# Performance work log

Hardware: AMD Instinct MI355X
Metric: run time of the kernel (lower is better)

Reference implementation:

```python
import jax, jax.numpy as jnp
import numpy as np

T = 16000        # signal length
N1 = 120         # first-order filters (J=12, Q=10)
NPSI2 = 14       # second-order filterbank size (Q2=1)
NPAIR = 553      # second-order coefficients -> 120 + 553 = 673 channels
SUB1 = 8         # subsample U1 before order 2
T2 = T // SUB1   # 2000
STR1 = 1000      # lowpass stride at length T  -> 16 output samples
STR2 = T2 // (T // STR1)  # 125 -> 16 output samples
LOG_EPS = 1e-6
BN_EPS = 1e-5


def _gauss_hat(N, xi, sigma):
    om = np.arange(N) / N
    return np.exp(-((om - xi) ** 2) / (2.0 * sigma ** 2)).astype(np.float32)


def _filterbank():
    Q = 10.0
    xi1 = 0.45 * 2.0 ** (-np.arange(N1) / Q)
    sig1 = np.maximum(xi1 * 0.1, 2.0 / T)
    psi1 = np.stack([_gauss_hat(T, x, s) for x, s in zip(xi1, sig1)])
    phi1 = _gauss_hat(T, 0.0, 0.4 / STR1)
    xi2 = 0.45 * 2.0 ** (-np.arange(NPSI2, dtype=np.float64))
    sig2 = np.maximum(xi2 * 0.2, 2.0 / T2)
    psi2 = np.stack([_gauss_hat(T2, x, s) for x, s in zip(xi2, sig2)])
    phi2 = _gauss_hat(T2, 0.0, 0.4 / STR2)
    pairs = [(i, j) for i in range(N1) for j in range(NPSI2) if xi2[j] < xi1[i] / 2.0]
    pairs = pairs[:NPAIR]
    assert len(pairs) == NPAIR
    pi1 = np.array([p[0] for p in pairs], np.int32)
    pi2 = np.array([p[1] for p in pairs], np.int32)
    return psi1, phi1, psi2, phi2, pi1, pi2


def setup_inputs():
    key = jax.random.key(0)
    ks = jax.random.split(key, 8)
    psi1, phi1, psi2, phi2, pi1, pi2 = _filterbank()
    B = 32
    inp = {
        "x": jax.random.normal(ks[0], (B, 1, T), jnp.float32),
        "psi1_hat": jnp.asarray(psi1),
        "phi1_hat": jnp.asarray(phi1),
        "psi2_hat": jnp.asarray(psi2),
        "phi2_hat": jnp.asarray(phi2),
        "gamma": jnp.ones((673,), jnp.float32),
        "beta": jnp.zeros((673,), jnp.float32),
        "W1": jax.random.normal(ks[1], (300, 673), jnp.float32) * 0.04,
        "b1": jnp.zeros((300,), jnp.float32),
        "W2": jax.random.normal(ks[2], (90, 300), jnp.float32) * 0.06,
        "b2": jnp.zeros((90,), jnp.float32),
        "W3": jax.random.normal(ks[3], (35, 90), jnp.float32) * 0.1,
        "b3": jnp.zeros((35,), jnp.float32),
        "pair_i1": jnp.asarray(pi1),
        "pair_i2": jnp.asarray(pi2),
    }
    return inp


def reference(x, psi1_hat, phi1_hat, psi2_hat, phi2_hat, gamma, beta,
              W1, b1, W2, b2, W3, b3, pair_i1, pair_i2):
    xs = x.squeeze(1)                                       # [B, T]
    Xf = jnp.fft.fft(xs)                                    # [B, T] c64
    # --- order 1: wavelet conv (freq-domain), modulus ---
    U1 = jnp.abs(jnp.fft.ifft(Xf[:, None, :] * psi1_hat[None]))        # [B, N1, T]
    # S1 = lowpass(U1) subsampled to 16 samples
    S1 = jnp.real(jnp.fft.ifft(jnp.fft.fft(U1) * phi1_hat))[..., ::STR1]  # [B, N1, 16]
    # --- order 2 on subsampled U1 ---
    U1sf = jnp.fft.fft(U1[..., ::SUB1])                     # [B, N1, T2]
    U2 = jnp.abs(jnp.fft.ifft(U1sf[:, pair_i1, :] * psi2_hat[pair_i2]))  # [B, NPAIR, T2]
    S2 = jnp.real(jnp.fft.ifft(jnp.fft.fft(U2) * phi2_hat))[..., ::STR2]  # [B, NPAIR, 16]
    S = jnp.concatenate([S1, S2], axis=1)                   # [B, 673, 16]
    # log-abs + temporal mean pooling
    f = jnp.mean(jnp.log(jnp.abs(S) + LOG_EPS), axis=-1)    # [B, 673]
    # BatchNorm1d (training mode: batch statistics)
    mu = jnp.mean(f, axis=0)
    var = jnp.var(f, axis=0)
    f = (f - mu) / jnp.sqrt(var + BN_EPS) * gamma + beta
    # MLP head
    h = jax.nn.relu(f @ W1.T + b1)
    h = jax.nn.relu(h @ W2.T + b2)
    return jax.nn.log_softmax(h @ W3.T + b3, axis=-1)
```

## Files before the change

kernel.cpp:

```cpp
#include <hip/hip_runtime.h>
#include <math.h>

typedef float2 cf;

__device__ __forceinline__ cf cadd(cf a, cf b){ return make_float2(a.x+b.x, a.y+b.y); }
__device__ __forceinline__ cf csub(cf a, cf b){ return make_float2(a.x-b.x, a.y-b.y); }
__device__ __forceinline__ cf cmul(cf a, cf b){ return make_float2(a.x*b.x - a.y*b.y, a.x*b.y + a.y*b.x); }

__device__ __forceinline__ int SW(int i){ return i ^ ((i>>4)&15); }
#define AT(x) s[SW(x)]
#define WFENCE asm volatile("" ::: "memory")


template<int N, int L, bool INV>
__device__ __forceinline__ void stage_r2(cf* __restrict__ s, const cf* __restrict__ tw, int tid, int nt){
  constexpr int Ls = L/2, nbf = N/2, tws = 16000/L;
  for (int q = tid; q < nbf; q += nt){
    int blk = q / Ls, j = q - blk*Ls;
    int base = blk*L + j;
    cf w1 = tw[tws*j]; if (INV) w1.y = -w1.y;
    if (!INV){
      cf a = AT(base), b = AT(base+Ls);
      AT(base) = cadd(a,b);
      AT(base+Ls) = cmul(csub(a,b), w1);
    } else {
      cf a = AT(base), b = cmul(AT(base+Ls), w1);
      AT(base) = cadd(a,b);
      AT(base+Ls) = csub(a,b);
    }
  }
}

template<int N, int L, bool INV>
__device__ __forceinline__ void stage_r4(cf* __restrict__ s, const cf* __restrict__ tw, int tid, int nt){
  constexpr int Ls = L/4, nbf = N/4, tws = 16000/L;
  for (int q = tid; q < nbf; q += nt){
    int blk = q / Ls, j = q - blk*Ls;
    int base = blk*L + j;
    cf w1 = tw[tws*j]; if (INV) w1.y = -w1.y;
    cf w2 = cmul(w1,w1), w3 = cmul(w2,w1);
    if (!INV){
      cf y0=AT(base), y1=AT(base+Ls), y2=AT(base+2*Ls), y3=AT(base+3*Ls);
      cf t0=cadd(y0,y2), t1=csub(y0,y2), t2=cadd(y1,y3), t3=csub(y1,y3);
      AT(base)      = cadd(t0,t2);
      AT(base+Ls)   = cmul(make_float2(t1.x + t3.y, t1.y - t3.x), w1);
      AT(base+2*Ls) = cmul(csub(t0,t2), w2);
      AT(base+3*Ls) = cmul(make_float2(t1.x - t3.y, t1.y + t3.x), w3);
    } else {
      cf z0=AT(base);
      cf z1=cmul(AT(base+Ls),   w1);
      cf z2=cmul(AT(base+2*Ls), w2);
      cf z3=cmul(AT(base+3*Ls), w3);
      cf t0=cadd(z0,z2), t1=csub(z0,z2), t2=cadd(z1,z3), t3=csub(z1,z3);
      AT(base)      = cadd(t0,t2);
      AT(base+Ls)   = make_float2(t1.x - t3.y, t1.y + t3.x);
      AT(base+2*Ls) = csub(t0,t2);
      AT(base+3*Ls) = make_float2(t1.x + t3.y, t1.y - t3.x);
    }
  }
}

template<int N, int L, bool INV>
__device__ __forceinline__ void stage_r5(cf* __restrict__ s, const cf* __restrict__ tw, int tid, int nt){
  constexpr int Ls = L/5, nbf = N/5, tws = 16000/L;
  const float C1 = 0.30901699437494742f, S1c = 0.95105651629515357f;
  const float C2 = -0.80901699437494745f, S2c = 0.58778525229247314f;
  for (int q = tid; q < nbf; q += nt){
    int blk = q / Ls, j = q - blk*Ls;
    int base = blk*L + j;
    cf w1 = tw[tws*j]; if (INV) w1.y = -w1.y;
    cf w2 = cmul(w1,w1), w3 = cmul(w2,w1), w4 = cmul(w2,w2);
    if (!INV){
      cf y0=AT(base), y1=AT(base+Ls), y2=AT(base+2*Ls), y3=AT(base+3*Ls), y4=AT(base+4*Ls);
      cf t1=cadd(y1,y4), t2=csub(y1,y4), t3=cadd(y2,y3), t4=csub(y2,y3);
      cf z0 = cadd(y0, cadd(t1,t3));
      cf m1 = make_float2(y0.x + C1*t1.x + C2*t3.x, y0.y + C1*t1.y + C2*t3.y);
      cf m2 = make_float2(y0.x + C2*t1.x + C1*t3.x, y0.y + C2*t1.y + C1*t3.y);
      cf wa = make_float2(S1c*t2.x + S2c*t4.x, S1c*t2.y + S2c*t4.y);
      cf wb = make_float2(S2c*t2.x - S1c*t4.x, S2c*t2.y - S1c*t4.y);
      cf o1 = make_float2(m1.x + wa.y, m1.y - wa.x);
      cf o4 = make_float2(m1.x - wa.y, m1.y + wa.x);
      cf o2 = make_float2(m2.x + wb.y, m2.y - wb.x);
      cf o3 = make_float2(m2.x - wb.y, m2.y + wb.x);
      AT(base) = z0;
      AT(base+Ls)   = cmul(o1,w1);
      AT(base+2*Ls) = cmul(o2,w2);
      AT(base+3*Ls) = cmul(o3,w3);
      AT(base+4*Ls) = cmul(o4,w4);
    } else {
      cf z0=AT(base);
      cf z1=cmul(AT(base+Ls),   w1);
      cf z2=cmul(AT(base+2*Ls), w2);
      cf z3=cmul(AT(base+3*Ls), w3);
      cf z4=cmul(AT(base+4*Ls), w4);
      cf t1=cadd(z1,z4), t2=csub(z1,z4), t3=cadd(z2,z3), t4=csub(z2,z3);
      cf y0 = cadd(z0, cadd(t1,t3));
      cf m1 = make_float2(z0.x + C1*t1.x + C2*t3.x, z0.y + C1*t1.y + C2*t3.y);
      cf m2 = make_float2(z0.x + C2*t1.x + C1*t3.x, z0.y + C2*t1.y + C1*t3.y);
      cf wa = make_float2(S1c*t2.x + S2c*t4.x, S1c*t2.y + S2c*t4.y);
      cf wb = make_float2(S2c*t2.x - S1c*t4.x, S2c*t2.y - S1c*t4.y);
      AT(base)      = y0;
      AT(base+Ls)   = make_float2(m1.x - wa.y, m1.y + wa.x);
      AT(base+2*Ls) = make_float2(m2.x - wb.y, m2.y + wb.x);
      AT(base+3*Ls) = make_float2(m2.x + wb.y, m2.y - wb.x);
      AT(base+4*Ls) = make_float2(m1.x + wa.y, m1.y - wa.x);
    }
  }
}

template<bool INV>
__device__ void fft16000(cf* s, const cf* tw, int tid, int nt){
  if (!INV){
    stage_r5<16000,16000,false>(s,tw,tid,nt); __syncthreads();
    stage_r5<16000, 3200,false>(s,tw,tid,nt); __syncthreads();
    stage_r5<16000,  640,false>(s,tw,tid,nt); __syncthreads();
    stage_r4<16000,  128,false>(s,tw,tid,nt); __syncthreads();
    stage_r4<16000,   32,false>(s,tw,tid,nt); __syncthreads();
    stage_r4<16000,    8,false>(s,tw,tid,nt); __syncthreads();
    stage_r2<16000,    2,false>(s,tw,tid,nt); __syncthreads();
  } else {
    stage_r2<16000,    2,true >(s,tw,tid,nt); __syncthreads();
    stage_r4<16000,    8,true >(s,tw,tid,nt); __syncthreads();
    stage_r4<16000,   32,true >(s,tw,tid,nt); __syncthreads();
    stage_r4<16000,  128,true >(s,tw,tid,nt); __syncthreads();
    stage_r5<16000,  640,true >(s,tw,tid,nt); __syncthreads();
    stage_r5<16000, 3200,true >(s,tw,tid,nt); __syncthreads();
    stage_r5<16000,16000,true >(s,tw,tid,nt); __syncthreads();
  }
}

template<bool INV>
__device__ void fft2000(cf* s, const cf* tw, int tid, int nt){
  if (!INV){
    stage_r5<2000,2000,false>(s,tw,tid,nt); __syncthreads();
    stage_r5<2000, 400,false>(s,tw,tid,nt); __syncthreads();
    stage_r5<2000,  80,false>(s,tw,tid,nt); __syncthreads();
    stage_r4<2000,  16,false>(s,tw,tid,nt); __syncthreads();
    stage_r4<2000,   4,false>(s,tw,tid,nt); __syncthreads();
  } else {
    stage_r4<2000,   4,true >(s,tw,tid,nt); __syncthreads();
    stage_r4<2000,  16,true >(s,tw,tid,nt); __syncthreads();
    stage_r5<2000,  80,true >(s,tw,tid,nt); __syncthreads();
    stage_r5<2000, 400,true >(s,tw,tid,nt); __syncthreads();
    stage_r5<2000,2000,true >(s,tw,tid,nt); __syncthreads();
  }
}

__device__ void fft8000i(cf* s, const cf* tw, int tid, int nt){
  stage_r4<8000,   4,true>(s,tw,tid,nt); __syncthreads();
  stage_r4<8000,  16,true>(s,tw,tid,nt); __syncthreads();
  stage_r4<8000,  64,true>(s,tw,tid,nt); __syncthreads();
  stage_r5<8000, 320,true>(s,tw,tid,nt); __syncthreads();
  stage_r5<8000,1600,true>(s,tw,tid,nt); __syncthreads();
  stage_r5<8000,8000,true>(s,tw,tid,nt); __syncthreads();
}
__device__ void fft4000i(cf* s, const cf* tw, int tid, int nt){
  stage_r2<4000,   2,true>(s,tw,tid,nt); __syncthreads();
  stage_r4<4000,   8,true>(s,tw,tid,nt); __syncthreads();
  stage_r4<4000,  32,true>(s,tw,tid,nt); __syncthreads();
  stage_r5<4000, 160,true>(s,tw,tid,nt); __syncthreads();
  stage_r5<4000, 800,true>(s,tw,tid,nt); __syncthreads();
  stage_r5<4000,4000,true>(s,tw,tid,nt); __syncthreads();
}
__device__ void fft1000i(cf* s, const cf* tw, int tid, int nt){
  stage_r2<1000,   2,true>(s,tw,tid,nt); __syncthreads();
  stage_r4<1000,   8,true>(s,tw,tid,nt); __syncthreads();
  stage_r5<1000,  40,true>(s,tw,tid,nt); __syncthreads();
  stage_r5<1000, 200,true>(s,tw,tid,nt); __syncthreads();
  stage_r5<1000,1000,true>(s,tw,tid,nt); __syncthreads();
}
__device__ void fft500i(cf* s, const cf* tw, int tid, int nt){
  stage_r4<500,  4,true>(s,tw,tid,nt); __syncthreads();
  stage_r5<500, 20,true>(s,tw,tid,nt); __syncthreads();
  stage_r5<500,100,true>(s,tw,tid,nt); __syncthreads();
  stage_r5<500,500,true>(s,tw,tid,nt); __syncthreads();
}
__device__ __forceinline__ void fft250w(cf* s, const cf* tw, int lane){
  stage_r2<250,  2,true>(s,tw,lane,64); WFENCE;
  stage_r5<250, 10,true>(s,tw,lane,64); WFENCE;
  stage_r5<250, 50,true>(s,tw,lane,64); WFENCE;
  stage_r5<250,250,true>(s,tw,lane,64); WFENCE;
}

__device__ __forceinline__ int pos16000(int k){
  int k0=k%5; k/=5; int k1=k%5; k/=5; int k2=k%5; k/=5;
  int k3=k&3; k>>=2; int k4=k&3; k>>=2; int k5=k&3; k>>=2;
  return k0*3200 + k1*640 + k2*128 + k3*32 + k4*8 + k5*2 + k;
}
__device__ __forceinline__ int pos8000(int k){
  int k0=k%5; k/=5; int k1=k%5; k/=5; int k2=k%5; k/=5;
  int k3=k&3, k4=(k>>2)&3, k5=k>>4;
  return k0*1600 + k1*320 + k2*64 + k3*16 + k4*4 + k5;
}
__device__ __forceinline__ int pos4000(int k){
  int k0=k%5; k/=5; int k1=k%5; k/=5; int k2=k%5; k/=5;
  int k3=k&3, k4=(k>>2)&3, k5=k>>4;
  return k0*800 + k1*160 + k2*32 + k3*8 + k4*2 + k5;
}
__device__ __forceinline__ int pos2000(int k){
  int k0=k%5; k/=5; int k1=k%5; k/=5; int k2=k%5; k/=5;
  int k3=k&3, k4=k>>2;
  return k0*400 + k1*80 + k2*16 + k3*4 + k4;
}
__device__ __forceinline__ int pos1000(int k){
  int k0=k%5; k/=5; int k1=k%5; k/=5; int k2=k%5; k/=5;
  int k3=k&3, k4=k>>2;
  return k0*200 + k1*40 + k2*8 + k3*2 + k4;
}
__device__ __forceinline__ int pos500(int k){
  int k0=k%5; k/=5; int k1=k%5; k/=5; int k2=k%5; k/=5;
  return k0*100 + k1*20 + k2*4 + k;
}
__device__ __forceinline__ int pos250(int k){
  int k0=k%5; k/=5; int k1=k%5; k/=5; int k2=k%5; k/=5;
  return k0*50 + k1*10 + k2*2 + k;
}

template<int M> __device__ __forceinline__ int posM(int k){
  if constexpr (M==16000) return pos16000(k);
  else if constexpr (M==8000) return pos8000(k);
  else if constexpr (M==4000) return pos4000(k);
  else return pos2000(k);
}
template<int M> __device__ __forceinline__ void fftM_inv(cf* s, const cf* tw, int tid, int nt){
  if constexpr (M==16000) fft16000<true>(s,tw,tid,nt);
  else if constexpr (M==8000) fft8000i(s,tw,tid,nt);
  else if constexpr (M==4000) fft4000i(s,tw,tid,nt);
  else fft2000<true>(s,tw,tid,nt);
}


__global__ void k_tw(cf* __restrict__ tw){
  int j = blockIdx.x*blockDim.x + threadIdx.x;
  if (j < 16000){
    double a = -6.283185307179586476925286766559 * (double)j / 16000.0;
    tw[j] = make_float2((float)cos(a), (float)sin(a));
  }
}

__global__ void k_btab(const float* __restrict__ phi1, const float* __restrict__ phi2,
                       float* __restrict__ h1g, float* __restrict__ h2g){
  int i = blockIdx.x*blockDim.x + threadIdx.x;
  const double TWO_PI = 6.283185307179586476925286766559;
  if (i < 5201){
    int d = i - 2600;
    double a = 0.0;
    for (int k = 0; k < 64; ++k) a += (double)phi1[k]*cos(TWO_PI*(double)(k*d)/16000.0);
    h1g[i] = (float)(a/16000.0 - (double)phi1[0]/32000.0);
  } else if (i == 5201){
    h1g[5201] = phi1[0]*(1.f/32000.f);
  } else if (i < 5202 + 661){
    int j = i - 5202; int d = j - 330;
    double a = 0.0;
    for (int k = 0; k < 64; ++k) a += (double)phi2[k]*cos(TWO_PI*(double)(k*d)/2000.0);
    h2g[j] = (float)(a/2000.0 - (double)phi2[0]/4000.0);
  } else if (i == 5202 + 661){
    h2g[661] = phi2[0]*(1.f/4000.f);
  }
}

__global__ __launch_bounds__(1024) void k_classify(const int* __restrict__ pi2,
                                                   int* __restrict__ list5, int* __restrict__ list4){
  __shared__ int w5[16], w4[16];
  int p = threadIdx.x;
  for (int t = p; t < 493; t += 1024) list5[t] = 0;
  for (int t = p; t < 60;  t += 1024) list4[t] = 0;
  bool valid = p < 553;
  int j2 = valid ? pi2[p] : 99;
  bool f5 = valid && (j2 >= 5);
  bool f4 = valid && (j2 < 5);
  unsigned long long m5 = __ballot(f5);
  unsigned long long m4 = __ballot(f4);
  int lane = p & 63, wid = p >> 6;
  if (lane == 0){ w5[wid] = __popcll(m5); w4[wid] = __popcll(m4); }
  __syncthreads();
  if (valid){
    int b5 = 0, b4 = 0;
    for (int w = 0; w < wid; ++w){ b5 += w5[w]; b4 += w4[w]; }
    unsigned long long lm = (1ull << lane) - 1ull;
    if (f5) list5[b5 + __popcll(m5 & lm)] = p;
    if (f4) list4[b4 + __popcll(m4 & lm)] = p;
  }
}

__global__ __launch_bounds__(1024) void k_fftx(const float* __restrict__ x, cf* __restrict__ Xf,
                                               const cf* __restrict__ tw){
  extern __shared__ cf s[];
  int b = blockIdx.x;
  int tid = threadIdx.x, nt = blockDim.x;
  for (int n = tid; n < 16000; n += nt) AT(n) = make_float2(x[b*16000 + n], 0.f);
  __syncthreads();
  fft16000<false>(s, tw, tid, nt);
  for (int k = tid; k < 16000; k += nt) Xf[b*16000 + k] = AT(pos16000(k));
}

template<int M, int ST, int NF, int I0, int NT>
__global__ __launch_bounds__(NT) void kf(const cf* __restrict__ Xf, const float* __restrict__ psi1,
                                         const float* __restrict__ h1g, const cf* __restrict__ tw,
                                         cf* __restrict__ U1sf, float* __restrict__ S1){
  extern __shared__ cf s[];
  constexpr int NW = NT/64;
  int b = blockIdx.x / NF;
  int i = I0 + (blockIdx.x - b*NF);
  int tid = threadIdx.x, wid = tid>>6, lane = tid&63;
  double x1 = 0.45 * exp2((double)(-i) / 10.0);
  double kc = 16000.0 * x1;
  double sg = fmax(1600.0 * x1, 2.0);
  int k0 = max(0, (int)floor(kc - 6.5*sg));
  int k1 = min(16000, (int)ceil(kc + 6.5*sg) + 1);
  int W = k1 - k0;
  for (int n = tid; n < M; n += NT) s[n] = make_float2(0.f, 0.f);
  __syncthreads();
  const cf* X = Xf + (size_t)b*16000 + k0;
  const float* P = psi1 + (size_t)i*16000 + k0;
  for (int j = tid; j < W; j += NT){
    cf v = X[j]; float pf = P[j];
    int pp = posM<M>(j);
    AT(pp) = make_float2(v.x*pf, v.y*pf);
  }
  __syncthreads();
  fftM_inv<M>(s, tw, tid, NT);
  constexpr int R = (M + NT - 1)/NT;
  float mreg[R]; float tsum = 0.f;
  const float inv = 1.f/16000.f;
  #pragma unroll
  for (int r = 0; r < R; ++r){
    int n = tid + r*NT;
    if (n < M){ cf v = AT(n); mreg[r] = sqrtf(v.x*v.x + v.y*v.y)*inv; tsum += mreg[r]; }
    else mreg[r] = 0.f;
  }
  float* fl; float* part;
  if constexpr (M == 2000){ fl = (float*)(s + 2000); part = fl + 2000; }
  else { fl = (float*)s; part = (float*)(s + M); }
  if constexpr (M != 2000) __syncthreads();
  #pragma unroll
  for (int r = 0; r < R; ++r){ int n = tid + r*NT; if (n < M) fl[n] = mreg[r]; }
  #pragma unroll
  for (int o = 32; o > 0; o >>= 1) tsum += __shfl_xor(tsum, o);
  if (lane == 0) part[wid] = tsum;
  __syncthreads();
  if (tid == 0){ float tt = 0.f; for (int w = 0; w < NW; ++w) tt += part[w]; part[NW] = tt; }
  __syncthreads();
  float stot = part[NW];
  float c1 = h1g[5201];
  for (int t = wid; t < 16; t += NW){
    int mlo = (1000*t - 2600)/ST;
    int mhi = (1000*t + 2600)/ST;
    float acc = 0.f;
    for (int m = mlo + lane; m <= mhi; m += 64){
      int mm = m; if (mm < 0) mm += M; else if (mm >= M) mm -= M;
      acc = fmaf(fl[mm], h1g[1000*t - m*ST + 2600], acc);
    }
    #pragma unroll
    for (int o = 32; o > 0; o >>= 1) acc += __shfl_xor(acc, o);
    if (lane == 0) S1[((size_t)b*120 + i)*16 + t] = (float)ST*(acc + c1*stot);
  }
  if constexpr (M != 2000){
    constexpr int K = 8/ST;
    float d0 = fl[tid*K];
    float d1 = 0.f;
    { int m2 = tid + 1024; if (m2 < 2000) d1 = fl[m2*K]; }
    __syncthreads();
    AT(tid) = make_float2(d0, 0.f);
    { int m2 = tid + 1024; if (m2 < 2000) AT(m2) = make_float2(d1, 0.f); }
    __syncthreads();
  } else {
    for (int n = tid; n < 2000; n += NT) AT(n) = make_float2(fl[n], 0.f);
    __syncthreads();
  }
  fft2000<false>(s, tw, tid, NT);
  cf* out = U1sf + ((size_t)b*120 + i)*2000;
  for (int k = tid; k < 2000; k += NT) out[k] = AT(pos2000(k));
}

__global__ __launch_bounds__(256) void k_sec5(const cf* __restrict__ U1sf, const float* __restrict__ psi2,
                                              const float* __restrict__ h2g, const cf* __restrict__ tw,
                                              const int* __restrict__ pi1, const int* __restrict__ pi2,
                                              const int* __restrict__ list5, float* __restrict__ S2){
  __shared__ cf sall[4*256];
  __shared__ float flall[4*256];
  int wid = threadIdx.x >> 6, lane = threadIdx.x & 63;
  int q = blockIdx.x*4 + wid;
  int p = list5[q >> 5];
  int b = q & 31;
  int i1 = pi1[p], j2 = pi2[p];
  cf* s = sall + wid*256;
  float* fl2 = flall + wid*256;
  double xc = exp2((double)(-j2));
  double kc = 900.0*xc, sg = fmax(180.0*xc, 2.0);
  int k0 = max(0, (int)floor(kc - 6.5*sg));
  int k1 = min(2000, (int)ceil(kc + 6.5*sg) + 1);
  int W = k1 - k0;
  for (int n = lane; n < 256; n += 64) s[n] = make_float2(0.f, 0.f);
  WFENCE;
  const cf* U = U1sf + (size_t)(b*120 + i1)*2000 + k0;
  const float* F = psi2 + j2*2000 + k0;
  for (int j = lane; j < W; j += 64){
    cf v = U[j]; float f = F[j];
    AT(pos250(j)) = make_float2(v.x*f, v.y*f);
  }
  WFENCE;
  fft250w(s, tw, lane);
  float tsum = 0.f;
  #pragma unroll
  for (int r = 0; r < 4; ++r){
    int n = lane + r*64;
    if (n < 250){
      cf v = AT(n);
      float mg = sqrtf(v.x*v.x + v.y*v.y)*(1.f/2000.f);
      fl2[n] = mg; tsum += mg;
    }
  }
  WFENCE;
  #pragma unroll
  for (int o = 32; o > 0; o >>= 1) tsum += __shfl_xor(tsum, o);
  float stot = tsum;
  float c2 = h2g[661];
  float* S2o = S2 + (size_t)(b*553 + p)*16;
  for (int t = 0; t < 16; ++t){
    int mlo = (125*t - 330 + 7) >> 3;
    int mhi = (125*t + 330) >> 3;
    float acc = 0.f;
    for (int m = mlo + lane; m <= mhi; m += 64){
      int mm = m; if (mm < 0) mm += 250; else if (mm >= 250) mm -= 250;
      acc = fmaf(fl2[mm], h2g[125*t - m*8 + 330], acc);
    }
    #pragma unroll
    for (int o = 32; o > 0; o >>= 1) acc += __shfl_xor(acc, o);
    if (lane == 0) S2o[t] = 8.f*(acc + c2*stot);
  }
}

__global__ __launch_bounds__(128) void k_secbig(const cf* __restrict__ U1sf, const float* __restrict__ psi2,
                                                const float* __restrict__ h2g, const cf* __restrict__ tw,
                                                const int* __restrict__ pi1, const int* __restrict__ pi2,
                                                const int* __restrict__ list4, float* __restrict__ S2){
  extern __shared__ cf s[];
  float* fl2 = (float*)(s + 2000);
  float* part = fl2 + 2000;
  int p = list4[blockIdx.x >> 5];
  int b = blockIdx.x & 31;
  int tid = threadIdx.x, wid = tid>>6, lane = tid&63;
  int i1 = pi1[p], j2 = pi2[p];
  int M2, s2l;
  if (j2 == 4){ M2 = 500;  s2l = 2; }
  else if (j2 == 3){ M2 = 1000; s2l = 1; }
  else { M2 = 2000; s2l = 0; }
  int ST2 = 1 << s2l;
  double xc = exp2((double)(-j2));
  double kc = 900.0*xc, sg = fmax(180.0*xc, 2.0);
  int k0 = max(0, (int)floor(kc - 6.5*sg));
  int k1 = min(2000, (int)ceil(kc + 6.5*sg) + 1);
  int W = k1 - k0;
  int M2r = (M2 + 15) & ~15;
  for (int n = tid; n < M2r; n += 128) s[n] = make_float2(0.f, 0.f);
  __syncthreads();
  const cf* U = U1sf + (size_t)(b*120 + i1)*2000 + k0;
  const float* F = psi2 + j2*2000 + k0;
  for (int j = tid; j < W; j += 128){
    cf v = U[j]; float f = F[j];
    int pp;
    if (M2 == 500) pp = pos500(j);
    else if (M2 == 1000) pp = pos1000(j);
    else pp = pos2000(j);
    AT(pp) = make_float2(v.x*f, v.y*f);
  }
  __syncthreads();
  if (M2 == 500) fft500i(s, tw, tid, 128);
  else if (M2 == 1000) fft1000i(s, tw, tid, 128);
  else fft2000<true>(s, tw, tid, 128);
  float tsum = 0.f;
  for (int n = tid; n < M2; n += 128){
    cf v = AT(n);
    float mg = sqrtf(v.x*v.x + v.y*v.y)*(1.f/2000.f);
    fl2[n] = mg; tsum += mg;
  }
  #pragma unroll
  for (int o = 32; o > 0; o >>= 1) tsum += __shfl_xor(tsum, o);
  if (lane == 0) part[wid] = tsum;
  __syncthreads();
  float stot = part[0] + part[1];
  float c2 = h2g[661];
  float* S2o = S2 + (size_t)(b*553 + p)*16;
  for (int r = 0; r < 8; ++r){
    int t = wid + (r<<1);
    int mlo = (125*t - 330 + ST2 - 1) >> s2l;
    int mhi = (125*t + 330) >> s2l;
    float acc = 0.f;
    for (int m = mlo + lane; m <= mhi; m += 64){
      int mm = m; if (mm < 0) mm += M2; else if (mm >= M2) mm -= M2;
      acc = fmaf(fl2[mm], h2g[125*t - m*ST2 + 330], acc);
    }
    #pragma unroll
    for (int o = 32; o > 0; o >>= 1) acc += __shfl_xor(acc, o);
    if (lane == 0) S2o[t] = (float)ST2*(acc + c2*stot);
  }
}

__global__ __launch_bounds__(64) void k_fbn(const float* __restrict__ S1, const float* __restrict__ S2,
                                            const float* __restrict__ g, const float* __restrict__ be,
                                            float* __restrict__ fn){
  int j = blockIdx.x;
  int b = threadIdx.x;
  float f = 0.f;
  if (b < 32){
    const float* src = (j < 120) ? (S1 + (b*120 + j)*16) : (S2 + (b*553 + (j-120))*16);
    float acc = 0.f;
    #pragma unroll
    for (int t = 0; t < 16; ++t) acc += logf(fabsf(src[t]) + 1e-6f);
    f = acc * (1.f/16.f);
  }
  float mu = f;
  #pragma unroll
  for (int o = 16; o > 0; o >>= 1) mu += __shfl_xor(mu, o);
  mu *= (1.f/32.f);
  float d = f - mu;
  float v = d*d;
  #pragma unroll
  for (int o = 16; o > 0; o >>= 1) v += __shfl_xor(v, o);
  v *= (1.f/32.f);
  float is = g[j] / sqrtf(v + 1e-5f);
  if (b < 32) fn[b*673 + j] = d*is + be[j];
}

__global__ __launch_bounds__(512) void k_mlp1(const float* __restrict__ fn,
                                              const float* __restrict__ W1, const float* __restrict__ b1,
                                              float* __restrict__ h1o){
  int task = blockIdx.x*8 + (threadIdx.x >> 6);
  int lane = threadIdx.x & 63;
  if (task >= 32*300) return;
  int b = task / 300, r = task - b*300;
  const float* f = fn + b*673;
  const float* w = W1 + r*673;
  float acc = 0.f;
  for (int k = lane; k < 673; k += 64) acc = fmaf(f[k], w[k], acc);
  #pragma unroll
  for (int o = 32; o > 0; o >>= 1) acc += __shfl_down(acc, o);
  if (lane == 0) h1o[b*300 + r] = fmaxf(acc + b1[r], 0.f);
}

__global__ __launch_bounds__(512) void k_mlp2(const float* __restrict__ h1,
                                              const float* __restrict__ W2, const float* __restrict__ b2,
                                              float* __restrict__ h2o){
  int task = blockIdx.x*8 + (threadIdx.x >> 6);
  int lane = threadIdx.x & 63;
  if (task >= 32*90) return;
  int b = task / 90, r = task - b*90;
  const float* h = h1 + b*300;
  const float* w = W2 + r*300;
  float acc = 0.f;
  for (int k = lane; k < 300; k += 64) acc = fmaf(h[k], w[k], acc);
  #pragma unroll
  for (int o = 32; o > 0; o >>= 1) acc += __shfl_down(acc, o);
  if (lane == 0) h2o[b*90 + r] = fmaxf(acc + b2[r], 0.f);
}

__global__ __launch_bounds__(256) void k_mlp3(const float* __restrict__ h2,
                                              const float* __restrict__ W3, const float* __restrict__ b3,
                                              float* __restrict__ out){
  __shared__ float lg[35];
  int b = blockIdx.x;
  int tid = threadIdx.x, wid = tid >> 6, lane = tid & 63;
  for (int r = wid; r < 35; r += 4){
    float acc = 0.f;
    for (int k = lane; k < 90; k += 64) acc = fmaf(h2[b*90 + k], W3[r*90 + k], acc);
    #pragma unroll
    for (int o = 32; o > 0; o >>= 1) acc += __shfl_down(acc, o);
    if (lane == 0) lg[r] = acc + b3[r];
  }
  __syncthreads();
  if (tid < 64){
    float v = (tid < 35) ? lg[tid] : -1e30f;
    float mx = v;
    #pragma unroll
    for (int o = 32; o > 0; o >>= 1) mx = fmaxf(mx, __shfl_xor(mx, o));
    float e = (tid < 35) ? expf(v - mx) : 0.f;
    float se = e;
    #pragma unroll
    for (int o = 32; o > 0; o >>= 1) se += __shfl_xor(se, o);
    if (tid < 35) out[b*35 + tid] = v - mx - logf(se);
  }
}


extern "C" void kernel_launch(void* const* d_in, const int* in_sizes, int n_in,
                              void* d_out, int out_size, void* d_ws, size_t ws_size,
                              hipStream_t stream){
  const float* x     = (const float*)d_in[0];
  const float* psi1  = (const float*)d_in[1];
  const float* phi1  = (const float*)d_in[2];
  const float* psi2  = (const float*)d_in[3];
  const float* phi2  = (const float*)d_in[4];
  const float* gamma = (const float*)d_in[5];
  const float* beta  = (const float*)d_in[6];
  const float* W1    = (const float*)d_in[7];
  const float* b1    = (const float*)d_in[8];
  const float* W2    = (const float*)d_in[9];
  const float* b2    = (const float*)d_in[10];
  const float* W3    = (const float*)d_in[11];
  const float* b3    = (const float*)d_in[12];
  const int*   pi1   = (const int*)d_in[13];
  const int*   pi2   = (const int*)d_in[14];

  char* ws = (char*)d_ws;
  constexpr size_t o_tw = 0;
  constexpr size_t o_Xf = o_tw + (size_t)16000*sizeof(cf);
  constexpr size_t o_U  = o_Xf + (size_t)32*16000*sizeof(cf);
  constexpr size_t o_S1 = o_U  + (size_t)3840*2000*sizeof(cf);
  constexpr size_t o_S2 = o_S1 + (size_t)3840*16*sizeof(float);
  constexpr size_t o_l5 = o_S2 + (size_t)17696*16*sizeof(float);
  constexpr size_t o_l4 = o_l5 + (size_t)512*sizeof(int);
  constexpr size_t o_fn = o_l4 + (size_t)64*sizeof(int);
  constexpr size_t o_h1 = o_fn + (size_t)32*673*sizeof(float);
  constexpr size_t o_h2 = o_h1 + (size_t)5202*sizeof(float);
  constexpr size_t o_m1 = o_h2 + (size_t)662*sizeof(float);
  constexpr size_t o_m2 = o_m1 + (size_t)32*300*sizeof(float);

  cf*    tw    = (cf*)(ws + o_tw);
  cf*    Xf    = (cf*)(ws + o_Xf);
  cf*    U1sf  = (cf*)(ws + o_U);
  float* S1b   = (float*)(ws + o_S1);
  float* S2b   = (float*)(ws + o_S2);
  int*   list5 = (int*)(ws + o_l5);
  int*   list4 = (int*)(ws + o_l4);
  float* fnbuf = (float*)(ws + o_fn);
  float* h1g   = (float*)(ws + o_h1);
  float* h2g   = (float*)(ws + o_h2);
  float* m1buf = (float*)(ws + o_m1);
  float* m2buf = (float*)(ws + o_m2);

  hipFuncSetAttribute((const void*)k_fftx, hipFuncAttributeMaxDynamicSharedMemorySize, 131072);
  hipFuncSetAttribute((const void*)kf<16000,1,13, 0,1024>, hipFuncAttributeMaxDynamicSharedMemorySize, 131072);
  hipFuncSetAttribute((const void*)kf< 8000,2,10,13,1024>, hipFuncAttributeMaxDynamicSharedMemorySize, 131072);

  k_tw<<<63, 256, 0, stream>>>(tw);
  k_btab<<<23, 256, 0, stream>>>(phi1, phi2, h1g, h2g);
  k_classify<<<1, 1024, 0, stream>>>(pi2, list5, list4);
  k_fftx<<<32, 1024, 128000, stream>>>(x, Xf, tw);
  kf<16000,1,13, 0,1024><<<32*13, 1024, 16000*8 + 17*4, stream>>>(Xf, psi1, h1g, tw, U1sf, S1b);
  kf< 8000,2,10,13,1024><<<32*10, 1024,  8000*8 + 17*4, stream>>>(Xf, psi1, h1g, tw, U1sf, S1b);
  kf< 4000,4,10,23,1024><<<32*10, 1024,  4000*8 + 17*4, stream>>>(Xf, psi1, h1g, tw, U1sf, S1b);
  kf< 2000,8,87,33, 256><<<32*87,  256,  2000*8 + 2000*4 + 5*4, stream>>>(Xf, psi1, h1g, tw, U1sf, S1b);
  k_sec5<<<(493*32)/4, 256, 0, stream>>>(U1sf, psi2, h2g, tw, pi1, pi2, list5, S2b);
  k_secbig<<<60*32, 128, 2000*8 + 2000*4 + 4*4, stream>>>(U1sf, psi2, h2g, tw, pi1, pi2, list4, S2b);
  k_fbn<<<673, 64, 0, stream>>>(S1b, S2b, gamma, beta, fnbuf);
  k_mlp1<<<1200, 512, 0, stream>>>(fnbuf, W1, b1, m1buf);
  k_mlp2<<<360, 512, 0, stream>>>(m1buf, W2, b2, m2buf);
  k_mlp3<<<32, 256, 0, stream>>>(m2buf, W3, b3, (float*)d_out);
}
```

Before: 383.1 us.

## Shrink first-order IFFT length for narrowband filters and truncate U1sf output

Narrow-bandwidth first-order filters (i>=43) now run their inverse FFT at reduced lengths (1000, 500, 250, 200, 125) instead of 2000. This works because their spectra fit in fewer bins, and the lowpass and forward FFT strides are rescaled to match. Small sizes use one wavefront per signal with wave-level fences instead of block barriers. U1sf writes are limited to the bins up to a per-filter bandwidth bound (devB) that order-2 needs, cutting global stores. The aliasing assumptions are approximate, so there is some accuracy risk, and unwritten U1sf bins stay stale.

```diff
diff --git a/kernel.cpp b/kernel.cpp
--- a/kernel.cpp
+++ b/kernel.cpp
@@ -11,6 +11,15 @@
 #define AT(x) s[SW(x)]
 #define WFENCE asm volatile("" ::: "memory")
 
+__device__ __forceinline__ int idivf(int a, int b){ return (a >= 0) ? a/b : -((-a + b - 1)/b); }
+__device__ __forceinline__ int idivc(int a, int b){ return (a >= 0) ? (a + b - 1)/b : -((-a)/b); }
+
+__device__ __forceinline__ int devB(int i){
+  int jm = i/10 + 2;
+  double kc = 900.0*exp2((double)(-jm));
+  double sg = fmax(180.0*exp2((double)(-jm)), 2.0);
+  return min(2000, (int)ceil(kc + 6.5*sg) + 1);
+}
 
 template<int N, int L, bool INV>
 __device__ __forceinline__ void stage_r2(cf* __restrict__ s, const cf* __restrict__ tw, int tid, int nt){
@@ -169,18 +178,73 @@
   stage_r5<1000, 200,true>(s,tw,tid,nt); __syncthreads();
   stage_r5<1000,1000,true>(s,tw,tid,nt); __syncthreads();
 }
+__device__ void fft1000f(cf* s, const cf* tw, int tid, int nt){
+  stage_r5<1000,1000,false>(s,tw,tid,nt); __syncthreads();
+  stage_r5<1000, 200,false>(s,tw,tid,nt); __syncthreads();
+  stage_r5<1000,  40,false>(s,tw,tid,nt); __syncthreads();
+  stage_r4<1000,   8,false>(s,tw,tid,nt); __syncthreads();
+  stage_r2<1000,   2,false>(s,tw,tid,nt); __syncthreads();
+}
 __device__ void fft500i(cf* s, const cf* tw, int tid, int nt){
   stage_r4<500,  4,true>(s,tw,tid,nt); __syncthreads();
   stage_r5<500, 20,true>(s,tw,tid,nt); __syncthreads();
   stage_r5<500,100,true>(s,tw,tid,nt); __syncthreads();
   stage_r5<500,500,true>(s,tw,tid,nt); __syncthreads();
 }
+
 __device__ __forceinline__ void fft250w(cf* s, const cf* tw, int lane){
   stage_r2<250,  2,true>(s,tw,lane,64); WFENCE;
   stage_r5<250, 10,true>(s,tw,lane,64); WFENCE;
   stage_r5<250, 50,true>(s,tw,lane,64); WFENCE;
   stage_r5<250,250,true>(s,tw,lane,64); WFENCE;
 }
+template<int M, bool INV>
+__device__ __forceinline__ void fft_w(cf* s, const cf* tw, int lane){
+  if constexpr (M==500){
+    if constexpr (!INV){
+      stage_r5<500,500,false>(s,tw,lane,64); WFENCE;
+      stage_r5<500,100,false>(s,tw,lane,64); WFENCE;
+      stage_r5<500, 20,false>(s,tw,lane,64); WFENCE;
+      stage_r4<500,  4,false>(s,tw,lane,64); WFENCE;
+    } else {
+      stage_r4<500,  4,true>(s,tw,lane,64); WFENCE;
+      stage_r5<500, 20,true>(s,tw,lane,64); WFENCE;
+      stage_r5<500,100,true>(s,tw,lane,64); WFENCE;
+      stage_r5<500,500,true>(s,tw,lane,64); WFENCE;
+    }
+  } else if constexpr (M==250){
+    if constexpr (!INV){
+      stage_r5<250,250,false>(s,tw,lane,64); WFENCE;
+      stage_r5<250, 50,false>(s,tw,lane,64); WFENCE;
+      stage_r5<250, 10,false>(s,tw,lane,64); WFENCE;
+      stage_r2<250,  2,false>(s,tw,lane,64); WFENCE;
+    } else {
+      fft250w(s,tw,lane);
+    }
+  } else if constexpr (M==200){
+    if constexpr (!INV){
+      stage_r5<200,200,false>(s,tw,lane,64); WFENCE;
+      stage_r5<200, 40,false>(s,tw,lane,64); WFENCE;
+      stage_r4<200,  8,false>(s,tw,lane,64); WFENCE;
+      stage_r2<200,  2,false>(s,tw,lane,64); WFENCE;
+    } else {
+      stage_r2<200,  2,true>(s,tw,lane,64); WFENCE;
+      stage_r4<200,  8,true>(s,tw,lane,64); WFENCE;
+      stage_r5<200, 40,true>(s,tw,lane,64); WFENCE;
+      stage_r5<200,200,true>(s,tw,lane,64); WFENCE;
+    }
+  } else {
+    if constexpr (!INV){
+      stage_r5<125,125,false>(s,tw,lane,64); WFENCE;
+      stage_r5<125, 25,false>(s,tw,lane,64); WFENCE;
+      stage_r5<125,  5,false>(s,tw,lane,64); WFENCE;
+    } else {
+      stage_r5<125,  5,true>(s,tw,lane,64); WFENCE;
+      stage_r5<125, 25,true>(s,tw,lane,64); WFENCE;
+      stage_r5<125,125,true>(s,tw,lane,64); WFENCE;
+    }
+  }
+}
 
 __device__ __forceinline__ int pos16000(int k){
   int k0=k%5; k/=5; int k1=k%5; k/=5; int k2=k%5; k/=5;
@@ -214,6 +278,15 @@
 __device__ __forceinline__ int pos250(int k){
   int k0=k%5; k/=5; int k1=k%5; k/=5; int k2=k%5; k/=5;
   return k0*50 + k1*10 + k2*2 + k;
+}
+__device__ __forceinline__ int pos200(int k){
+  int k0=k%5; k/=5; int k1=k%5; k/=5;
+  int k2=k&3, k3=k>>2;
+  return k0*40 + k1*8 + k2*2 + k3;
+}
+__device__ __forceinline__ int pos125(int k){
+  int k0=k%5; k/=5; int k1=k%5; k/=5;
+  return k0*25 + k1*5 + k;
 }
 
 template<int M> __device__ __forceinline__ int posM(int k){
@@ -221,6 +294,12 @@
   else if constexpr (M==8000) return pos8000(k);
   else if constexpr (M==4000) return pos4000(k);
   else return pos2000(k);
+}
+template<int M> __device__ __forceinline__ int posS(int k){
+  if constexpr (M==500) return pos500(k);
+  else if constexpr (M==250) return pos250(k);
+  else if constexpr (M==200) return pos200(k);
+  else return pos125(k);
 }
 template<int M> __device__ __forceinline__ void fftM_inv(cf* s, const cf* tw, int tid, int nt){
   if constexpr (M==16000) fft16000<true>(s,tw,tid,nt);
@@ -329,10 +408,9 @@
     if (n < M){ cf v = AT(n); mreg[r] = sqrtf(v.x*v.x + v.y*v.y)*inv; tsum += mreg[r]; }
     else mreg[r] = 0.f;
   }
-  float* fl; float* part;
-  if constexpr (M == 2000){ fl = (float*)(s + 2000); part = fl + 2000; }
-  else { fl = (float*)s; part = (float*)(s + M); }
-  if constexpr (M != 2000) __syncthreads();
+  float* fl = (float*)s;
+  float* part = (float*)(s + M);
+  __syncthreads();
   #pragma unroll
   for (int r = 0; r < R; ++r){ int n = tid + r*NT; if (n < M) fl[n] = mreg[r]; }
   #pragma unroll
@@ -355,22 +433,142 @@
     for (int o = 32; o > 0; o >>= 1) acc += __shfl_xor(acc, o);
     if (lane == 0) S1[((size_t)b*120 + i)*16 + t] = (float)ST*(acc + c1*stot);
   }
-  if constexpr (M != 2000){
-    constexpr int K = 8/ST;
-    float d0 = fl[tid*K];
-    float d1 = 0.f;
-    { int m2 = tid + 1024; if (m2 < 2000) d1 = fl[m2*K]; }
-    __syncthreads();
-    AT(tid) = make_float2(d0, 0.f);
-    { int m2 = tid + 1024; if (m2 < 2000) AT(m2) = make_float2(d1, 0.f); }
-    __syncthreads();
-  } else {
-    for (int n = tid; n < 2000; n += NT) AT(n) = make_float2(fl[n], 0.f);
-    __syncthreads();
-  }
+  constexpr int K = 8/ST;
+  float d0 = fl[tid*K];
+  float d1 = 0.f;
+  { int m2 = tid + 1024; if (m2 < 2000) d1 = fl[m2*K]; }
+  __syncthreads();
+  AT(tid) = make_float2(d0, 0.f);
+  { int m2 = tid + 1024; if (m2 < 2000) AT(m2) = make_float2(d1, 0.f); }
+  __syncthreads();
   fft2000<false>(s, tw, tid, NT);
+  int B = devB(i);
   cf* out = U1sf + ((size_t)b*120 + i)*2000;
-  for (int k = tid; k < 2000; k += NT) out[k] = AT(pos2000(k));
+  for (int k = tid; k < B; k += NT) out[k] = AT(pos2000(k));
+}
+
+template<int M, int ST, int NF, int I0>
+__global__ __launch_bounds__(256) void k_nb(const cf* __restrict__ Xf, const float* __restrict__ psi1,
+                                            const float* __restrict__ h1g, const cf* __restrict__ tw,
+                                            cf* __restrict__ U1sf, float* __restrict__ S1){
+  extern __shared__ cf s[];
+  float* fl = (float*)(s + M);
+  float* part = fl + M;
+  int b = blockIdx.x / NF;
+  int i = I0 + (blockIdx.x - b*NF);
+  int tid = threadIdx.x, wid = tid>>6, lane = tid&63;
+  double x1 = 0.45 * exp2((double)(-i)/10.0);
+  double kc = 16000.0*x1, sg = fmax(1600.0*x1, 2.0);
+  int k0 = max(0,(int)floor(kc-6.5*sg));
+  int k1 = min(16000,(int)ceil(kc+6.5*sg)+1);
+  int W = k1-k0;
+  for (int n = tid; n < M; n += 256) s[n] = make_float2(0.f,0.f);
+  __syncthreads();
+  const cf* X = Xf + (size_t)b*16000 + k0;
+  const float* P = psi1 + (size_t)i*16000 + k0;
+  for (int j = tid; j < W; j += 256){
+    cf v = X[j]; float pf = P[j];
+    int pp = (M==2000) ? pos2000(j) : pos1000(j);
+    AT(pp) = make_float2(v.x*pf, v.y*pf);
+  }
+  __syncthreads();
+  if constexpr (M==2000) fft2000<true>(s,tw,tid,256); else fft1000i(s,tw,tid,256);
+  float tsum = 0.f;
+  for (int n = tid; n < M; n += 256){
+    cf v = AT(n);
+    float mg = sqrtf(v.x*v.x+v.y*v.y)*(1.f/16000.f);
+    fl[n] = mg; tsum += mg;
+  }
+  #pragma unroll
+  for (int o=32;o>0;o>>=1) tsum += __shfl_xor(tsum,o);
+  if (lane==0) part[wid] = tsum;
+  __syncthreads();
+  float stot = part[0]+part[1]+part[2]+part[3];
+  float c1 = h1g[5201];
+  float* S1o = S1 + ((size_t)b*120+i)*16;
+  for (int r = 0; r < 4; ++r){
+    int t = wid + 4*r;
+    int mlo = idivc(1000*t-2600,ST), mhi = idivf(1000*t+2600,ST);
+    float acc = 0.f;
+    for (int m = mlo+lane; m <= mhi; m += 64){
+      int mm = m; if (mm<0) mm+=M; else if (mm>=M) mm-=M;
+      acc = fmaf(fl[mm], h1g[1000*t - m*ST + 2600], acc);
+    }
+    #pragma unroll
+    for (int o=32;o>0;o>>=1) acc += __shfl_xor(acc,o);
+    if (lane==0) S1o[t] = (float)ST*(acc + c1*stot);
+  }
+  __syncthreads();
+  for (int n = tid; n < M; n += 256) AT(n) = make_float2(fl[n], 0.f);
+  __syncthreads();
+  if constexpr (M==2000) fft2000<false>(s,tw,tid,256); else fft1000f(s,tw,tid,256);
+  int B = devB(i);
+  const float sc = 2000.f/(float)M;
+  cf* out = U1sf + ((size_t)b*120+i)*2000;
+  for (int k = tid; k < B; k += 256){
+    cf v = AT((M==2000)?pos2000(k):pos1000(k));
+    out[k] = make_float2(v.x*sc, v.y*sc);
+  }
+}
+
+template<int M, int SPAD, int ST, int NF, int I0, int WPB>
+__global__ __launch_bounds__(WPB*64) void k_nw(const cf* __restrict__ Xf, const float* __restrict__ psi1,
+                                               const float* __restrict__ h1g, const cf* __restrict__ tw,
+                                               cf* __restrict__ U1sf, float* __restrict__ S1){
+  extern __shared__ cf sh[];
+  int wid = threadIdx.x >> 6, lane = threadIdx.x & 63;
+  int q = blockIdx.x*WPB + wid;
+  int filt = q >> 5, b = q & 31;
+  int i = I0 + filt;
+  cf* s = sh + wid*SPAD;
+  float* fl = ((float*)(sh + WPB*SPAD)) + wid*SPAD;
+  double x1 = 0.45 * exp2((double)(-i)/10.0);
+  double kc = 16000.0*x1, sg = fmax(1600.0*x1, 2.0);
+  int k0 = max(0,(int)floor(kc-6.5*sg));
+  int k1 = min(16000,(int)ceil(kc+6.5*sg)+1);
+  int W = k1-k0;
+  for (int n = lane; n < SPAD; n += 64) s[n] = make_float2(0.f,0.f);
+  WFENCE;
+  const cf* X = Xf + (size_t)b*16000 + k0;
+  const float* P = psi1 + (size_t)i*16000 + k0;
+  for (int j = lane; j < W; j += 64){
+    cf v = X[j]; float pf = P[j];
+    AT(posS<M>(j)) = make_float2(v.x*pf, v.y*pf);
+  }
+  WFENCE;
+  fft_w<M,true>(s,tw,lane);
+  float tsum = 0.f;
+  for (int n = lane; n < M; n += 64){
+    cf v = AT(n);
+    float mg = sqrtf(v.x*v.x+v.y*v.y)*(1.f/16000.f);
+    fl[n] = mg; tsum += mg;
+  }
+  WFENCE;
+  #pragma unroll
+  for (int o=32;o>0;o>>=1) tsum += __shfl_xor(tsum,o);
+  float c1 = h1g[5201];
+  float* S1o = S1 + ((size_t)b*120+i)*16;
+  for (int t = 0; t < 16; ++t){
+    int mlo = idivc(1000*t-2600,ST), mhi = idivf(1000*t+2600,ST);
+    float acc = 0.f;
+    for (int m = mlo+lane; m <= mhi; m += 64){
+      int mm = m; if (mm<0) mm+=M; else if (mm>=M) mm-=M;
+      acc = fmaf(fl[mm], h1g[1000*t - m*ST + 2600], acc);
+    }
+    #pragma unroll
+    for (int o=32;o>0;o>>=1) acc += __shfl_xor(acc,o);
+    if (lane==0) S1o[t] = (float)ST*(acc + c1*tsum);
+  }
+  for (int n = lane; n < M; n += 64) AT(n) = make_float2(fl[n], 0.f);
+  WFENCE;
+  fft_w<M,false>(s,tw,lane);
+  int B = devB(i);
+  const float sc = 2000.f/(float)M;
+  cf* out = U1sf + ((size_t)b*120+i)*2000;
+  for (int k = lane; k < B; k += 64){
+    cf v = AT(posS<M>(k));
+    out[k] = make_float2(v.x*sc, v.y*sc);
+  }
 }
 
 __global__ __launch_bounds__(256) void k_sec5(const cf* __restrict__ U1sf, const float* __restrict__ psi2,
@@ -640,7 +838,12 @@
   kf<16000,1,13, 0,1024><<<32*13, 1024, 16000*8 + 17*4, stream>>>(Xf, psi1, h1g, tw, U1sf, S1b);
   kf< 8000,2,10,13,1024><<<32*10, 1024,  8000*8 + 17*4, stream>>>(Xf, psi1, h1g, tw, U1sf, S1b);
   kf< 4000,4,10,23,1024><<<32*10, 1024,  4000*8 + 17*4, stream>>>(Xf, psi1, h1g, tw, U1sf, S1b);
-  kf< 2000,8,87,33, 256><<<32*87,  256,  2000*8 + 2000*4 + 5*4, stream>>>(Xf, psi1, h1g, tw, U1sf, S1b);
+  k_nb<2000, 8,10,33><<<32*10, 256, 2000*8 + 2000*4 + 5*4, stream>>>(Xf, psi1, h1g, tw, U1sf, S1b);
+  k_nb<1000,16,10,43><<<32*10, 256, 1000*8 + 1000*4 + 5*4, stream>>>(Xf, psi1, h1g, tw, U1sf, S1b);
+  k_nw< 500,512, 32,10,53,4><<< 80, 256, 4*512*12, stream>>>(Xf, psi1, h1g, tw, U1sf, S1b);
+  k_nw< 250,256, 64,10,63,8><<< 40, 512, 8*256*12, stream>>>(Xf, psi1, h1g, tw, U1sf, S1b);
+  k_nw< 200,208, 80,10,73,8><<< 40, 512, 8*208*12, stream>>>(Xf, psi1, h1g, tw, U1sf, S1b);
+  k_nw< 125,128,128,37,83,8><<<148, 512, 8*128*12, stream>>>(Xf, psi1, h1g, tw, U1sf, S1b);
   k_sec5<<<(493*32)/4, 256, 0, stream>>>(U1sf, psi2, h2g, tw, pi1, pi2, list5, S2b);
   k_secbig<<<60*32, 128, 2000*8 + 2000*4 + 4*4, stream>>>(U1sf, psi2, h2g, tw, pi1, pi2, list4, S2b);
   k_fbn<<<673, 64, 0, stream>>>(S1b, S2b, gamma, beta, fnbuf);
```

After: 392.4 us. 2.4% more time.
